# Performance work log

Measured on AMD Instinct MI355X. Metric: run time of the kernel, lower is better.

## Reference

```python
import jax, jax.numpy as jnp
import numpy as np

BETA = 0.99  # EMA momentum from init_kwargs
EPS = 1e-12  # torch F.normalize eps


def _normalize(v):
    # matches torch.nn.functional.normalize (L2, dim=-1, eps clamp)
    n = jnp.maximum(jnp.linalg.norm(v, axis=-1, keepdims=True), EPS)
    return v / n


def setup_inputs() -> dict:
    key = jax.random.key(0)
    k1, k2 = jax.random.split(key)
    x = jax.random.normal(k1, (16384, 1024), dtype=jnp.float32)
    group_features = jax.random.uniform(k2, (8192, 1024), dtype=jnp.float32)
    return {"x": x, "group_features": group_features}


def reference(x, group_features):
    n_groups = group_features.shape[0]
    # assign_groups: cosine-sim argmax (normalized copies; does NOT modify x used below)
    xn = _normalize(x)
    gn = _normalize(group_features)
    logits = xn @ gn.T                      # [B, G]
    assignments = jnp.argmax(logits, axis=-1)  # [B] int

    # bincount over groups
    counts = jax.ops.segment_sum(
        jnp.ones_like(assignments, dtype=jnp.int32), assignments, num_segments=n_groups
    )  # [G]

    # scale only groups that received at least one sample by beta
    gf = jnp.where((counts > 0)[:, None], group_features * BETA, group_features)

    # scatter-add EMA contribution: (1-beta) * mean-style sum of raw x per group
    per_sample = x / counts[assignments][:, None].astype(x.dtype)  # safe: count>=1 for assigned
    contrib = jax.ops.segment_sum(per_sample, assignments, num_segments=n_groups)  # [G, D]
    gf = gf + (1.0 - BETA) * contrib

    return _normalize(gf)
```

## Files before the change

### kernel.cpp

```cpp
#include <hip/hip_runtime.h>

#define B_N 16384
#define G_N 8192
#define D_N 1024
#define NT 96

typedef unsigned short u16;
typedef unsigned long long u64;
typedef __attribute__((ext_vector_type(8))) short short8;
typedef __attribute__((ext_vector_type(16))) float f32x16;

#define AS1 __attribute__((address_space(1)))
#define AS3 __attribute__((address_space(3)))


__global__ __launch_bounds__(256) void k_norms(const float* __restrict__ g,
                                               float* __restrict__ invn) {
    const int j = blockIdx.x;
    const int t = threadIdx.x;
    const float4 v = *reinterpret_cast<const float4*>(&g[(size_t)j * D_N + t * 4]);
    float s = v.x * v.x + v.y * v.y + v.z * v.z + v.w * v.w;
#pragma unroll
    for (int off = 32; off >= 1; off >>= 1) s += __shfl_down(s, off, 64);
    __shared__ float wsum[4];
    if ((t & 63) == 0) wsum[t >> 6] = s;
    __syncthreads();
    if (t == 0) {
        const float tot = wsum[0] + wsum[1] + wsum[2] + wsum[3];
        invn[j] = 1.0f / fmaxf(sqrtf(tot), 1e-12f);
    }
}

__global__ void k_counts(const u64* __restrict__ pk, int* __restrict__ counts) {
    const int i = blockIdx.x * blockDim.x + threadIdx.x;
    if (i < B_N) {
        const int a = 8191 - (int)(pk[i] & 0x1FFFull);
        atomicAdd(&counts[a], 1);
    }
}

__global__ __launch_bounds__(256) void k_scatter(const float* __restrict__ x,
                                                 const u64* __restrict__ pk,
                                                 const int* __restrict__ counts,
                                                 float* __restrict__ contrib) {
    const int i = blockIdx.x;
    const int a = 8191 - (int)(pk[i] & 0x1FFFull);
    const float scale = 1.0f / (float)counts[a];
    const int t = threadIdx.x;
    const float4 v = *reinterpret_cast<const float4*>(&x[(size_t)i * D_N + t * 4]);
    float* dst = &contrib[(size_t)a * D_N + t * 4];
    atomicAdd(dst + 0, v.x * scale);
    atomicAdd(dst + 1, v.y * scale);
    atomicAdd(dst + 2, v.z * scale);
    atomicAdd(dst + 3, v.w * scale);
}

__global__ __launch_bounds__(256) void k_finalize(const float* __restrict__ g,
                                                  const int* __restrict__ counts,
                                                  float* __restrict__ out) {
    const int j = blockIdx.x;
    const int t = threadIdx.x;
    const float sc = (counts[j] > 0) ? 0.99f : 1.0f;
    const float4 gv = *reinterpret_cast<const float4*>(&g[(size_t)j * D_N + t * 4]);
    const float4 cv = *reinterpret_cast<const float4*>(&out[(size_t)j * D_N + t * 4]);
    float4 gf;
    gf.x = sc * gv.x + 0.01f * cv.x;
    gf.y = sc * gv.y + 0.01f * cv.y;
    gf.z = sc * gv.z + 0.01f * cv.z;
    gf.w = sc * gv.w + 0.01f * cv.w;
    float s = gf.x * gf.x + gf.y * gf.y + gf.z * gf.z + gf.w * gf.w;
#pragma unroll
    for (int off = 32; off >= 1; off >>= 1) s += __shfl_down(s, off, 64);
    __shared__ float wsum[4];
    __shared__ float s_inv;
    if ((t & 63) == 0) wsum[t >> 6] = s;
    __syncthreads();
    if (t == 0) s_inv = 1.0f / fmaxf(sqrtf(wsum[0] + wsum[1] + wsum[2] + wsum[3]), 1e-12f);
    __syncthreads();
    gf.x *= s_inv; gf.y *= s_inv; gf.z *= s_inv; gf.w *= s_inv;
    *reinterpret_cast<float4*>(&out[(size_t)j * D_N + t * 4]) = gf;
}


__device__ inline u16 f2bf_rtn(float f) {
    unsigned u = __float_as_uint(f);
    unsigned r = u + 0x7fffu + ((u >> 16) & 1u);
    return (u16)(r >> 16);
}
__device__ inline float bf2f(u16 h) { return __uint_as_float(((unsigned)h) << 16); }

__global__ __launch_bounds__(256) void k_split_pack(const float* __restrict__ src,
                                                    u16* __restrict__ hi,
                                                    u16* __restrict__ lo) {
    const int id = blockIdx.x * 256 + threadIdx.x;
    const int brick = id >> 7, c = id & 127;
    const int mu = brick >> 5, tau = brick & 31;
    const int ks = c >> 6, lane = c & 63;
    const int row = mu * 32 + (lane & 31);
    const int k = tau * 32 + ks * 16 + (lane >> 5) * 8;
    const float* s = src + (size_t)row * D_N + k;
    const float4 v0 = *reinterpret_cast<const float4*>(s);
    const float4 v1 = *reinterpret_cast<const float4*>(s + 4);
    const float f[8] = {v0.x, v0.y, v0.z, v0.w, v1.x, v1.y, v1.z, v1.w};
    short8 h, l;
#pragma unroll
    for (int j = 0; j < 8; ++j) {
        const u16 hj = f2bf_rtn(f[j]);
        h[j] = (short)hj;
        l[j] = (short)f2bf_rtn(f[j] - bf2f(hj));
    }
    *reinterpret_cast<short8*>(hi + (size_t)id * 8) = h;
    *reinterpret_cast<short8*>(lo + (size_t)id * 8) = l;
}


#define MFMA_BLK() do {                                                                    \
    __builtin_amdgcn_s_setprio(1);                                                         \
    _Pragma("unroll")                                                                      \
    for (int m = 0; m < 4; ++m)                                                            \
        _Pragma("unroll")                                                                  \
        for (int ks = 0; ks < 2; ++ks)                                                     \
            _Pragma("unroll")                                                              \
            for (int n = 0; n < 4; ++n)                                                    \
                acc[m][n] = __builtin_amdgcn_mfma_f32_32x32x16_bf16(                       \
                    afr[m][ks], bfr[n][ks], acc[m][n], 0, 0, 0);                           \
    __builtin_amdgcn_s_setprio(0);                                                         \
} while (0)

#define READS(BUF) do {                                                                    \
    const u16* aB = lds + (BUF) * 16384 + aRd;                                             \
    const u16* bB = lds + (BUF) * 16384 + 8192 + bRd;                                      \
    _Pragma("unroll")                                                                      \
    for (int n = 0; n < 4; ++n)                                                            \
        _Pragma("unroll")                                                                  \
        for (int ks = 0; ks < 2; ++ks)                                                     \
            bfr[n][ks] = *reinterpret_cast<const short8*>(bB + n * 1024 + ks * 512);       \
    _Pragma("unroll")                                                                      \
    for (int m = 0; m < 4; ++m)                                                            \
        _Pragma("unroll")                                                                  \
        for (int ks = 0; ks < 2; ++ks)                                                     \
            afr[m][ks] = *reinterpret_cast<const short8*>(aB + m * 1024 + ks * 512);       \
} while (0)

#define BODY(P, BSTG, BRD) do {                                                            \
    STG((P) + 2, BSTG);                                                                    \
    READS(BRD);                                                                            \
    MFMA_BLK();                                                                            \
    asm volatile("s_waitcnt vmcnt(8)" ::: "memory");                                       \
    __builtin_amdgcn_s_barrier();                                                          \
} while (0)

__global__ __launch_bounds__(256, 1) void k_gemm_argmax(
    const u16* __restrict__ x_hi, const u16* __restrict__ x_lo,
    const u16* __restrict__ g_hi, const u16* __restrict__ g_lo,
    const float* __restrict__ invn, u64* __restrict__ pk) {

    __shared__ __align__(16) u16 lds[49152];

    const int bid = blockIdx.x;
    const int xcd = bid & 7, lcl = bid >> 3;
    const int mblk = xcd * 8 + ((lcl >> 3) & 7);
    const int nblk = (lcl & 7) + (lcl >> 6) * 8;
    const int mrow0 = mblk * 256, nrow0 = nblk * 256;

    const int tid = threadIdx.x;
    const int lane = tid & 63;
    const int w = tid >> 6;
    const int wr = w >> 1, wc = w & 1;
    const int l31 = lane & 31, l5 = lane >> 5;

    const int aRd = wr * 4096 + lane * 8;
    const int bRd = wc * 4096 + lane * 8;

    const int cOff = (tid & 127) * 8;
    const int hb = tid >> 7;
    const int wub = (tid & 192) * 8;
    const size_t aBase = ((size_t)(mblk * 8 + hb)) * 32768 + cOff;
    const size_t bBase = ((size_t)(nblk * 8 + hb)) * 32768 + cOff;

    auto STG = [&](int T, int buf) {
        const int Tc = T < NT ? T : NT - 1;
        const int term = Tc >> 5;
        const int tko = (Tc & 31) * 1024;
        const u16* xa = ((term == 1) ? x_lo : x_hi) + aBase + tko;
        const u16* gb = ((term == 2) ? g_lo : g_hi) + bBase + tko;
        u16* da = lds + buf * 16384 + wub;
        u16* db = da + 8192;
#pragma unroll
        for (int i = 0; i < 4; ++i)
            __builtin_amdgcn_global_load_lds((const AS1 void*)(xa + (size_t)i * 65536),
                                             (AS3 void*)(da + i * 2048), 16, 0, 0);
#pragma unroll
        for (int i = 0; i < 4; ++i)
            __builtin_amdgcn_global_load_lds((const AS1 void*)(gb + (size_t)i * 65536),
                                             (AS3 void*)(db + i * 2048), 16, 0, 0);
    };

    f32x16 acc[4][4];
#pragma unroll
    for (int m = 0; m < 4; ++m)
#pragma unroll
        for (int n = 0; n < 4; ++n)
#pragma unroll
            for (int r = 0; r < 16; ++r) acc[m][n][r] = 0.0f;

    short8 afr[4][2], bfr[4][2];

    STG(0, 0); STG(1, 1);
    asm volatile("s_waitcnt vmcnt(8)" ::: "memory");
    __builtin_amdgcn_s_barrier();

    for (int it = 0; it < 32; ++it) {
        const int q = it * 3;
        BODY(q,     2, 0);
        BODY(q + 1, 0, 1);
        BODY(q + 2, 1, 2);
    }

    float inv[4];
#pragma unroll
    for (int n = 0; n < 4; ++n) inv[n] = invn[nrow0 + wc * 128 + n * 32 + l31];

#pragma unroll
    for (int m = 0; m < 4; ++m) {
#pragma unroll
        for (int r = 0; r < 16; ++r) {
            u64 p = 0;
#pragma unroll
            for (int n = 0; n < 4; ++n) {
                const float v = acc[m][n][r] * inv[n];
                unsigned u = __float_as_uint(v);
                u ^= (u >> 31) ? 0xFFFFFFFFu : 0x80000000u;
                const int col = nrow0 + wc * 128 + n * 32 + l31;
                const u64 cand = ((u64)u << 13) | (unsigned)(8191 - col);
                p = (cand > p) ? cand : p;
            }
#pragma unroll
            for (int msk = 1; msk < 32; msk <<= 1) {
                const u64 o = __shfl_xor(p, msk, 64);
                p = (o > p) ? o : p;
            }
            if (l31 == 0) {
                const int row = mrow0 + wr * 128 + m * 32 + (r & 3) + 8 * (r >> 2) + 4 * l5;
                atomicMax(&pk[row], p);
            }
        }
    }
}


__global__ __launch_bounds__(256) void k_argmax_fp32(const float* __restrict__ x,
                                                     const float* __restrict__ g,
                                                     const float* __restrict__ invn,
                                                     int* __restrict__ assign) {
    __shared__ __align__(16) float As[32][68];
    __shared__ __align__(16) float Bs[32][68];
    const int t = threadIdx.x;
    const int tx = t & 15;
    const int ty = t >> 4;
    const int row0 = blockIdx.x * 64;
    const int r_a = t >> 3;
    const int c4 = t & 7;
    float bestv[4]; int besti[4];
#pragma unroll
    for (int i = 0; i < 4; ++i) { bestv[i] = -3.0e38f; besti[i] = 0; }
    for (int jt = 0; jt < G_N / 64; ++jt) {
        float acc[4][4] = {};
        for (int kt = 0; kt < D_N / 32; ++kt) {
#pragma unroll
            for (int p = 0; p < 2; ++p) {
                const int r = r_a + p * 32;
                const float4 va = *reinterpret_cast<const float4*>(&x[(size_t)(row0 + r) * D_N + kt * 32 + c4 * 4]);
                As[c4 * 4 + 0][r] = va.x; As[c4 * 4 + 1][r] = va.y; As[c4 * 4 + 2][r] = va.z; As[c4 * 4 + 3][r] = va.w;
                const float4 vb = *reinterpret_cast<const float4*>(&g[(size_t)(jt * 64 + r) * D_N + kt * 32 + c4 * 4]);
                Bs[c4 * 4 + 0][r] = vb.x; Bs[c4 * 4 + 1][r] = vb.y; Bs[c4 * 4 + 2][r] = vb.z; Bs[c4 * 4 + 3][r] = vb.w;
            }
            __syncthreads();
#pragma unroll
            for (int k = 0; k < 32; ++k) {
                const float4 a = *reinterpret_cast<const float4*>(&As[k][ty * 4]);
                const float4 b = *reinterpret_cast<const float4*>(&Bs[k][tx * 4]);
                const float av[4] = {a.x, a.y, a.z, a.w};
                const float bv[4] = {b.x, b.y, b.z, b.w};
#pragma unroll
                for (int i = 0; i < 4; ++i)
#pragma unroll
                    for (int jj = 0; jj < 4; ++jj) acc[i][jj] += av[i] * bv[jj];
            }
            __syncthreads();
        }
#pragma unroll
        for (int jj = 0; jj < 4; ++jj) {
            const int col = jt * 64 + tx * 4 + jj;
            const float s = invn[col];
#pragma unroll
            for (int i = 0; i < 4; ++i) {
                const float v = acc[i][jj] * s;
                if (v > bestv[i]) { bestv[i] = v; besti[i] = col; }
            }
        }
    }
#pragma unroll
    for (int m = 1; m < 16; m <<= 1) {
#pragma unroll
        for (int i = 0; i < 4; ++i) {
            const float ov = __shfl_xor(bestv[i], m, 64);
            const int oi = __shfl_xor(besti[i], m, 64);
            if (ov > bestv[i] || (ov == bestv[i] && oi < besti[i])) { bestv[i] = ov; besti[i] = oi; }
        }
    }
    if (tx == 0) {
#pragma unroll
        for (int i = 0; i < 4; ++i) assign[row0 + ty * 4 + i] = besti[i];
    }
}

__global__ void k_counts_i(const int* __restrict__ assign, int* __restrict__ counts) {
    const int i = blockIdx.x * blockDim.x + threadIdx.x;
    if (i < B_N) atomicAdd(&counts[assign[i]], 1);
}

__global__ __launch_bounds__(256) void k_scatter_i(const float* __restrict__ x,
                                                   const int* __restrict__ assign,
                                                   const int* __restrict__ counts,
                                                   float* __restrict__ contrib) {
    const int i = blockIdx.x;
    const int a = assign[i];
    const float scale = 1.0f / (float)counts[a];
    const int t = threadIdx.x;
    const float4 v = *reinterpret_cast<const float4*>(&x[(size_t)i * D_N + t * 4]);
    float* dst = &contrib[(size_t)a * D_N + t * 4];
    atomicAdd(dst + 0, v.x * scale);
    atomicAdd(dst + 1, v.y * scale);
    atomicAdd(dst + 2, v.z * scale);
    atomicAdd(dst + 3, v.w * scale);
}


extern "C" void kernel_launch(void* const* d_in, const int* in_sizes, int n_in,
                              void* d_out, int out_size, void* d_ws, size_t ws_size,
                              hipStream_t stream) {
    const float* x = (const float*)d_in[0];
    const float* g = (const float*)d_in[1];
    float* out = (float*)d_out;

    char* ws = (char*)d_ws;
    u16*  x_hi  = (u16*)(ws);
    u16*  x_lo  = (u16*)(ws + 33554432);
    u16*  g_hi  = (u16*)(ws + 67108864);
    u16*  g_lo  = (u16*)(ws + 83886080);
    float* invn = (float*)(ws + 100663296);
    int* counts = (int*)(ws + 100696064);
    u64*   pk   = (u64*)(ws + 100728832);
    const size_t need = 100859904;

    hipMemsetAsync(out, 0, (size_t)G_N * D_N * sizeof(float), stream);

    if (ws_size >= need) {
        hipMemsetAsync(counts, 0, (size_t)G_N * sizeof(int), stream);
        hipMemsetAsync(pk, 0, (size_t)B_N * sizeof(u64), stream);
        k_norms<<<G_N, 256, 0, stream>>>(g, invn);
        k_split_pack<<<B_N * D_N / 8 / 256, 256, 0, stream>>>(x, x_hi, x_lo);
        k_split_pack<<<G_N * D_N / 8 / 256, 256, 0, stream>>>(g, g_hi, g_lo);
        k_gemm_argmax<<<2048, 256, 0, stream>>>(x_hi, x_lo, g_hi, g_lo, invn, pk);
        k_counts<<<B_N / 256, 256, 0, stream>>>(pk, counts);
        k_scatter<<<B_N, 256, 0, stream>>>(x, pk, counts, out);
        k_finalize<<<G_N, 256, 0, stream>>>(g, counts, out);
    } else {
        float* invn_f = (float*)ws;
        int* assign_f = (int*)(ws + (size_t)G_N * 4);
        int* counts_f = (int*)(ws + (size_t)(G_N + B_N) * 4);
        hipMemsetAsync(counts_f, 0, (size_t)G_N * sizeof(int), stream);
        k_norms<<<G_N, 256, 0, stream>>>(g, invn_f);
        k_argmax_fp32<<<B_N / 64, 256, 0, stream>>>(x, g, invn_f, assign_f);
        k_counts_i<<<B_N / 256, 256, 0, stream>>>(assign_f, counts_f);
        k_scatter_i<<<B_N, 256, 0, stream>>>(x, assign_f, counts_f, out);
        k_finalize<<<G_N, 256, 0, stream>>>(g, counts_f, out);
    }
}
```

Before: 1.067 ms.

## Deepen LDS pipeline to 4 stages and double-buffer register fragments

Moves the GEMM main loop from a 3-stage to a 4-stage LDS ring buffer, raising shared memory from 96KB to 128KB. It also double-buffers the A/B register fragments, so LDS reads for the next k-step are issued before the MFMA block of the current one, with a sched_barrier to keep that order. The aim is to hide LDS read latency and global-load latency behind MFMA work. In exchange, register pressure rises (twice as many fragment registers alongside the 256-float accumulator), and the vmcnt(8) wait may no longer match the deeper prefetch.

```diff
diff --git a/kernel.cpp b/kernel.cpp
--- a/kernel.cpp
+++ b/kernel.cpp
@@ -114,7 +114,7 @@
 }
 
 
-#define MFMA_BLK() do {                                                                    \
+#define MFMA_BLK(S) do {                                                                   \
     __builtin_amdgcn_s_setprio(1);                                                         \
     _Pragma("unroll")                                                                      \
     for (int m = 0; m < 4; ++m)                                                            \
@@ -123,29 +123,30 @@
             _Pragma("unroll")                                                              \
             for (int n = 0; n < 4; ++n)                                                    \
                 acc[m][n] = __builtin_amdgcn_mfma_f32_32x32x16_bf16(                       \
-                    afr[m][ks], bfr[n][ks], acc[m][n], 0, 0, 0);                           \
+                    afr[S][m][ks], bfr[S][n][ks], acc[m][n], 0, 0, 0);                     \
     __builtin_amdgcn_s_setprio(0);                                                         \
 } while (0)
 
-#define READS(BUF) do {                                                                    \
+#define READS(BUF, S) do {                                                                 \
     const u16* aB = lds + (BUF) * 16384 + aRd;                                             \
     const u16* bB = lds + (BUF) * 16384 + 8192 + bRd;                                      \
     _Pragma("unroll")                                                                      \
     for (int n = 0; n < 4; ++n)                                                            \
         _Pragma("unroll")                                                                  \
         for (int ks = 0; ks < 2; ++ks)                                                     \
-            bfr[n][ks] = *reinterpret_cast<const short8*>(bB + n * 1024 + ks * 512);       \
+            bfr[S][n][ks] = *reinterpret_cast<const short8*>(bB + n * 1024 + ks * 512);    \
     _Pragma("unroll")                                                                      \
     for (int m = 0; m < 4; ++m)                                                            \
         _Pragma("unroll")                                                                  \
         for (int ks = 0; ks < 2; ++ks)                                                     \
-            afr[m][ks] = *reinterpret_cast<const short8*>(aB + m * 1024 + ks * 512);       \
+            afr[S][m][ks] = *reinterpret_cast<const short8*>(aB + m * 1024 + ks * 512);    \
 } while (0)
 
-#define BODY(P, BSTG, BRD) do {                                                            \
-    STG((P) + 2, BSTG);                                                                    \
-    READS(BRD);                                                                            \
-    MFMA_BLK();                                                                            \
+#define BODY(P, BRD, BSTG, SM, SR) do {                                                    \
+    READS(BRD, SR);                                                                        \
+    STG((P) + 3, BSTG);                                                                    \
+    __builtin_amdgcn_sched_barrier(0);                                                     \
+    MFMA_BLK(SM);                                                                          \
     asm volatile("s_waitcnt vmcnt(8)" ::: "memory");                                       \
     __builtin_amdgcn_s_barrier();                                                          \
 } while (0)
@@ -155,7 +156,7 @@
     const u16* __restrict__ g_hi, const u16* __restrict__ g_lo,
     const float* __restrict__ invn, u64* __restrict__ pk) {
 
-    __shared__ __align__(16) u16 lds[49152];
+    __shared__ __align__(16) u16 lds[65536];
 
     const int bid = blockIdx.x;
     const int xcd = bid & 7, lcl = bid >> 3;
@@ -204,17 +205,19 @@
 #pragma unroll
             for (int r = 0; r < 16; ++r) acc[m][n][r] = 0.0f;
 
-    short8 afr[4][2], bfr[4][2];
-
-    STG(0, 0); STG(1, 1);
+    short8 afr[2][4][2], bfr[2][4][2];
+
+    STG(0, 0); STG(1, 1); STG(2, 2);
     asm volatile("s_waitcnt vmcnt(8)" ::: "memory");
     __builtin_amdgcn_s_barrier();
-
-    for (int it = 0; it < 32; ++it) {
-        const int q = it * 3;
-        BODY(q,     2, 0);
-        BODY(q + 1, 0, 1);
-        BODY(q + 2, 1, 2);
+    READS(0, 0);
+
+    for (int it = 0; it < 24; ++it) {
+        const int p = it * 4;
+        BODY(p,     1, 3, 0, 1);
+        BODY(p + 1, 2, 0, 1, 0);
+        BODY(p + 2, 3, 1, 0, 1);
+        BODY(p + 3, 0, 2, 1, 0);
     }
 
     float inv[4];
```

New measurement: 1.063 ms. About the same (-0.3%).

## Double K-tile depth and switch from triple to double buffered LDS pipeline

Applied to the files above, without the earlier changes.

Each pipeline stage now covers 64 K-elements instead of 32, halving the number of stages and barriers. The LDS ring shrinks from three buffers to two larger ones, and each stage prefetches only one tile ahead with a full vmcnt(0) wait. This cuts barrier and loop overhead and doubles the MFMA work between syncs. The trade-off is less prefetch slack and a full drain of outstanding loads every stage, which could expose global load latency.

```diff
diff --git a/kernel.cpp b/kernel.cpp
--- a/kernel.cpp
+++ b/kernel.cpp
@@ -3,7 +3,7 @@
 #define B_N 16384
 #define G_N 8192
 #define D_N 1024
-#define NT 96
+#define NT 48
 
 typedef unsigned short u16;
 typedef unsigned long long u64;
@@ -117,36 +117,36 @@
 #define MFMA_BLK() do {                                                                    \
     __builtin_amdgcn_s_setprio(1);                                                         \
     _Pragma("unroll")                                                                      \
-    for (int m = 0; m < 4; ++m)                                                            \
+    for (int k4 = 0; k4 < 4; ++k4)                                                         \
         _Pragma("unroll")                                                                  \
-        for (int ks = 0; ks < 2; ++ks)                                                     \
+        for (int m = 0; m < 4; ++m)                                                        \
             _Pragma("unroll")                                                              \
             for (int n = 0; n < 4; ++n)                                                    \
                 acc[m][n] = __builtin_amdgcn_mfma_f32_32x32x16_bf16(                       \
-                    afr[m][ks], bfr[n][ks], acc[m][n], 0, 0, 0);                           \
+                    afr[m][k4], bfr[n][k4], acc[m][n], 0, 0, 0);                           \
     __builtin_amdgcn_s_setprio(0);                                                         \
 } while (0)
 
 #define READS(BUF) do {                                                                    \
-    const u16* aB = lds + (BUF) * 16384 + aRd;                                             \
-    const u16* bB = lds + (BUF) * 16384 + 8192 + bRd;                                      \
+    const u16* aB = lds + (BUF) * 32768 + wr * 8192 + lane * 8;                            \
+    const u16* bB = lds + (BUF) * 32768 + 16384 + wc * 8192 + lane * 8;                    \
     _Pragma("unroll")                                                                      \
-    for (int n = 0; n < 4; ++n)                                                            \
+    for (int k4 = 0; k4 < 4; ++k4) {                                                       \
+        const int ko = (k4 >> 1) * 1024 + (k4 & 1) * 512;                                  \
         _Pragma("unroll")                                                                  \
-        for (int ks = 0; ks < 2; ++ks)                                                     \
-            bfr[n][ks] = *reinterpret_cast<const short8*>(bB + n * 1024 + ks * 512);       \
-    _Pragma("unroll")                                                                      \
-    for (int m = 0; m < 4; ++m)                                                            \
+        for (int n = 0; n < 4; ++n)                                                        \
+            bfr[n][k4] = *reinterpret_cast<const short8*>(bB + n * 2048 + ko);             \
         _Pragma("unroll")                                                                  \
-        for (int ks = 0; ks < 2; ++ks)                                                     \
-            afr[m][ks] = *reinterpret_cast<const short8*>(aB + m * 1024 + ks * 512);       \
+        for (int m = 0; m < 4; ++m)                                                        \
+            afr[m][k4] = *reinterpret_cast<const short8*>(aB + m * 2048 + ko);             \
+    }                                                                                      \
 } while (0)
 
-#define BODY(P, BSTG, BRD) do {                                                            \
-    STG((P) + 2, BSTG);                                                                    \
+#define BODY(Q, BSTG, BRD) do {                                                            \
+    STG((Q) + 1, BSTG);                                                                    \
     READS(BRD);                                                                            \
     MFMA_BLK();                                                                            \
-    asm volatile("s_waitcnt vmcnt(8)" ::: "memory");                                       \
+    asm volatile("s_waitcnt vmcnt(0)" ::: "memory");                                       \
     __builtin_amdgcn_s_barrier();                                                          \
 } while (0)
 
@@ -155,7 +155,7 @@
     const u16* __restrict__ g_hi, const u16* __restrict__ g_lo,
     const float* __restrict__ invn, u64* __restrict__ pk) {
 
-    __shared__ __align__(16) u16 lds[49152];
+    __shared__ __align__(16) u16 lds[65536];
 
     const int bid = blockIdx.x;
     const int xcd = bid & 7, lcl = bid >> 3;
@@ -169,30 +169,26 @@
     const int wr = w >> 1, wc = w & 1;
     const int l31 = lane & 31, l5 = lane >> 5;
 
-    const int aRd = wr * 4096 + lane * 8;
-    const int bRd = wc * 4096 + lane * 8;
-
-    const int cOff = (tid & 127) * 8;
     const int hb = tid >> 7;
-    const int wub = (tid & 192) * 8;
-    const size_t aBase = ((size_t)(mblk * 8 + hb)) * 32768 + cOff;
-    const size_t bBase = ((size_t)(nblk * 8 + hb)) * 32768 + cOff;
+    const size_t aOff0 = (size_t)mblk * 262144 + hb * 1024 + (tid & 127) * 8;
+    const size_t bOff0 = (size_t)nblk * 262144 + hb * 1024 + (tid & 127) * 8;
+    const int dW = w * 512;
 
     auto STG = [&](int T, int buf) {
         const int Tc = T < NT ? T : NT - 1;
-        const int term = Tc >> 5;
-        const int tko = (Tc & 31) * 1024;
-        const u16* xa = ((term == 1) ? x_lo : x_hi) + aBase + tko;
-        const u16* gb = ((term == 2) ? g_lo : g_hi) + bBase + tko;
-        u16* da = lds + buf * 16384 + wub;
-        u16* db = da + 8192;
-#pragma unroll
-        for (int i = 0; i < 4; ++i)
-            __builtin_amdgcn_global_load_lds((const AS1 void*)(xa + (size_t)i * 65536),
+        const int term = Tc >> 4;
+        const size_t tko = (size_t)(Tc & 15) * 2048;
+        const u16* xa = ((term == 1) ? x_lo : x_hi) + aOff0 + tko;
+        const u16* gb = ((term == 2) ? g_lo : g_hi) + bOff0 + tko;
+        u16* da = lds + buf * 32768 + dW;
+        u16* db = da + 16384;
+#pragma unroll
+        for (int i = 0; i < 8; ++i)
+            __builtin_amdgcn_global_load_lds((const AS1 void*)(xa + (size_t)i * 32768),
                                              (AS3 void*)(da + i * 2048), 16, 0, 0);
 #pragma unroll
-        for (int i = 0; i < 4; ++i)
-            __builtin_amdgcn_global_load_lds((const AS1 void*)(gb + (size_t)i * 65536),
+        for (int i = 0; i < 8; ++i)
+            __builtin_amdgcn_global_load_lds((const AS1 void*)(gb + (size_t)i * 32768),
                                              (AS3 void*)(db + i * 2048), 16, 0, 0);
     };
 
@@ -204,17 +200,16 @@
 #pragma unroll
             for (int r = 0; r < 16; ++r) acc[m][n][r] = 0.0f;
 
-    short8 afr[4][2], bfr[4][2];
-
-    STG(0, 0); STG(1, 1);
-    asm volatile("s_waitcnt vmcnt(8)" ::: "memory");
+    short8 afr[4][4], bfr[4][4];
+
+    STG(0, 0);
+    asm volatile("s_waitcnt vmcnt(0)" ::: "memory");
     __builtin_amdgcn_s_barrier();
 
-    for (int it = 0; it < 32; ++it) {
-        const int q = it * 3;
-        BODY(q,     2, 0);
+    for (int it = 0; it < 24; ++it) {
+        const int q = it * 2;
+        BODY(q,     1, 0);
         BODY(q + 1, 0, 1);
-        BODY(q + 2, 1, 2);
     }
 
     float inv[4];
```

New measurement: 1.079 ms. Within noise of the previous version (+1.1%).
